# Performance work log

Measured on AMD Instinct MI355X. Metric: run time of the kernel, lower is better.

## Reference

```python
import jax, jax.numpy as jnp
import numpy as np

C_GMS = 0.0026  # constant c in the GMS map


def _median3(x):
    # 3x3 median with zero padding (matches kornia MedianBlur: conv2d-unfold
    # with zero padding, then median of the 9 values; odd count so torch's
    # lower-median == true median). x: [B,1,H,W]
    B, C, H, W = x.shape
    xp = jnp.pad(x, ((0, 0), (0, 0), (1, 1), (1, 1)))
    patches = jnp.stack(
        [xp[:, :, i:i + H, j:j + W] for i in range(3) for j in range(3)], axis=0
    )  # [9,B,1,H,W]
    return jnp.median(patches, axis=0)


def _prewitt(x):
    # fixed 2-channel Prewitt conv, VALID padding, then gradient magnitude
    Gx = jnp.array([[-1., 0., 1.], [-1., 0., 1.], [-1., 0., 1.]], dtype=x.dtype) / 3.0
    Gy = jnp.array([[1., 1., 1.], [0., 0., 0.], [-1., -1., -1.]], dtype=x.dtype) / 3.0
    k = jnp.stack([Gx, Gy])[:, None]  # [2,1,3,3] OIHW
    g = jax.lax.conv_general_dilated(
        x, k, window_strides=(1, 1), padding='VALID',
        dimension_numbers=('NCHW', 'OIHW', 'NCHW'))  # [B,2,H-2,W-2]
    return jnp.sqrt(jnp.sum(g * g, axis=1, keepdims=True))


def _gms_loss(Ii, Ir):
    x = jnp.mean(Ii, axis=1, keepdims=True)  # channel mean -> grayscale
    y = jnp.mean(Ir, axis=1, keepdims=True)
    gI = _prewitt(_median3(x))
    gR = _prewitt(_median3(y))
    gmap = (2.0 * gI * gR + C_GMS) / (gI * gI + gR * gR + C_GMS)
    return jnp.mean(1.0 - gmap)


def _avg_pool2(x):
    # avg_pool2d(kernel=2, stride=2)
    B, C, H, W = x.shape
    return x.reshape(B, C, H // 2, 2, W // 2, 2).mean(axis=(3, 5))


def setup_inputs() -> dict:
    key = jax.random.key(0)
    k1, k2 = jax.random.split(key)
    Ii = jax.random.uniform(k1, (16, 3, 512, 512), dtype=jnp.float32)
    Ir = jax.random.uniform(k2, (16, 3, 512, 512), dtype=jnp.float32)
    return {"Ii": Ii, "Ir": Ir}


def reference(Ii, Ir):
    total = _gms_loss(Ii, Ir)
    for _ in range(3):  # fixed 4-scale pyramid
        Ii = _avg_pool2(Ii)
        Ir = _avg_pool2(Ir)
        total = total + _gms_loss(Ii, Ir)
    return total / 4.0
```

## Files before the change

kernel.cpp:

```cpp
#include <hip/hip_runtime.h>

#define C_GMS 0.0026f

__device__ __forceinline__ float dppL(float x) {
    return __int_as_float(__builtin_amdgcn_mov_dpp(__float_as_int(x), 0x138, 0xf, 0xf, true));
}
__device__ __forceinline__ float dppR(float x) {
    return __int_as_float(__builtin_amdgcn_mov_dpp(__float_as_int(x), 0x130, 0xf, 0xf, true));
}
__device__ __forceinline__ float med3f(float a, float b, float c) {
    return __builtin_amdgcn_fmed3f(a, b, c);
}

template<bool RGB, bool POOL, int RC>
__global__ __launch_bounds__(256) void gms_scale_kernel(
    const float* __restrict__ srcX, const float* __restrict__ srcY,
    int H, int W, int nstrips, int nchunks,
    float* __restrict__ partial,
    float* __restrict__ dX, float* __restrict__ dY)
{
    const int lane = threadIdx.x & 63;
    const int u = blockIdx.x * 4 + (threadIdx.x >> 6);

    const int s  = u % nstrips;
    const int t1 = u / nstrips;
    const int k  = t1 % nchunks;
    const int b  = t1 / nchunks;

    const int c0 = 60 * s - 1;
    const int c  = c0 + lane;
    const int R0 = k * RC;
    const int iend = min(R0 + RC, H - 2);

    const int HW = H * W;
    const float* PX = srcX + (size_t)b * (RGB ? 3 * HW : HW);
    const float* PY = srcY + (size_t)b * (RGB ? 3 * HW : HW);
    const bool cok = (c >= 0) && (c < W);

    auto loadrow2 = [&](int r, float& vx, float& vy) {
        vx = 0.0f; vy = 0.0f;
        if (r >= 0 && r < H) {
            if (cok) {
                int o = r * W + c;
                if (RGB) {
                    vx = (PX[o] + PX[o + HW] + PX[o + 2 * HW]) * (1.0f / 3.0f);
                    vy = (PY[o] + PY[o + HW] + PY[o + 2 * HW]) * (1.0f / 3.0f);
                } else {
                    vx = PX[o];
                    vy = PY[o];
                }
            }
        }
    };

    auto medrow = [&](float ga, float gb, float gc, float& m, float& rs) {
        float lo = fminf(fminf(ga, gb), gc);
        float me = med3f(ga, gb, gc);
        float hi = fmaxf(fmaxf(ga, gb), gc);
        float lmax = fmaxf(fmaxf(dppL(lo), lo), dppR(lo));
        float mid  = med3f(dppL(me), me, dppR(me));
        float hmin = fminf(fminf(dppL(hi), hi), dppR(hi));
        m  = med3f(lmax, mid, hmin);
        rs = m + dppL(m) + dppR(m);
    };

    const int Hd = H >> 1, Wd = W >> 1;
    const int phalf = R0 >> 1;
    const int pend  = min(phalf + (RC >> 1), Hd);
    const bool poolLane = ((lane & 1) == 1) && (lane <= 59) && (c + 1 < W);

    auto dopool = [&](float bx, float cx, float by, float cy, int p) {
        if (!POOL) return;
        if (p < phalf || p >= pend) return;
        float ux = bx + cx, uy = by + cy;
        float hx = ux + dppR(ux);
        float hy = uy + dppR(uy);
        if (poolLane) {
            size_t o = ((size_t)b * Hd + p) * Wd + (c >> 1);
            dX[o] = hx * 0.25f;
            dY[o] = hy * 0.25f;
        }
    };

    float xa, ya, xb, yb, xc, yc, xd, yd, xe, ye;
    loadrow2(R0 - 1, xa, ya);
    loadrow2(R0,     xb, yb);
    loadrow2(R0 + 1, xc, yc);
    loadrow2(R0 + 2, xd, yd);
    loadrow2(R0 + 3, xe, ye);

    float mx0, mx1, mx2, rx0, rx1, rx2;
    float my0, my1, my2, ry0, ry1, ry2;
    medrow(xa, xb, xc, mx0, rx0); medrow(ya, yb, yc, my0, ry0);
    dopool(xb, xc, yb, yc, phalf);
    medrow(xb, xc, xd, mx1, rx1); medrow(yb, yc, yd, my1, ry1);
    medrow(xc, xd, xe, mx2, rx2); medrow(yc, yd, ye, my2, ry2);

    float gx2 = xd, gx3 = xe, gy2 = yd, gy3 = ye;

    const bool outLane = (lane >= 2) && (lane <= 61) && (c <= W - 2);
    float acc = 0.0f;

    for (int i = R0; i < iend; ++i) {
        float nx, ny;
        loadrow2(i + 4, nx, ny);

        float csx = mx0 + mx1 + mx2;
        float csy = my0 + my1 + my2;
        float Gxx = dppR(csx) - dppL(csx);
        float Gxy = dppR(csy) - dppL(csy);
        float Gyx = rx0 - rx2;
        float Gyy = ry0 - ry2;
        float gI = sqrtf(Gxx * Gxx + Gyx * Gyx) * (1.0f / 3.0f);
        float gR = sqrtf(Gxy * Gxy + Gyy * Gyy) * (1.0f / 3.0f);
        float gmap = (2.0f * gI * gR + C_GMS) / (gI * gI + gR * gR + C_GMS);
        if (outLane) acc += 1.0f - gmap;

        if (((i + 3) & 1) == 1) dopool(gx2, gx3, gy2, gy3, (i + 2) >> 1);

        float mxn, rxn, myn, ryn;
        medrow(gx2, gx3, nx, mxn, rxn);
        medrow(gy2, gy3, ny, myn, ryn);
        mx0 = mx1; mx1 = mx2; mx2 = mxn; rx0 = rx1; rx1 = rx2; rx2 = rxn;
        my0 = my1; my1 = my2; my2 = myn; ry0 = ry1; ry1 = ry2; ry2 = ryn;
        gx2 = gx3; gx3 = nx; gy2 = gy3; gy3 = ny;
    }

    for (int off = 32; off; off >>= 1) acc += __shfl_down(acc, off, 64);
    if (lane == 0) partial[u] = acc;
}

__global__ __launch_bounds__(256) void finalize_kernel(
    const float* __restrict__ P, int n0, int n1, int n2, int n3,
    float* __restrict__ out)
{
    const int tid = threadIdx.x;
    const double w0 = 1.0 / (4.0 * 16.0 * 510.0 * 510.0);
    const double w1 = 1.0 / (4.0 * 16.0 * 254.0 * 254.0);
    const double w2 = 1.0 / (4.0 * 16.0 * 126.0 * 126.0);
    const double w3 = 1.0 / (4.0 * 16.0 * 62.0 * 62.0);
    const int e0 = n0, e1 = e0 + n1, e2 = e1 + n2, e3 = e2 + n3;
    double v = 0.0;
    for (int i = tid; i < e3; i += 256) {
        double w = (i < e0) ? w0 : (i < e1) ? w1 : (i < e2) ? w2 : w3;
        v += (double)P[i] * w;
    }
    for (int off = 32; off; off >>= 1) v += __shfl_down(v, off, 64);
    __shared__ double wsum[4];
    int lane = tid & 63, wid = tid >> 6;
    if (lane == 0) wsum[wid] = v;
    __syncthreads();
    if (tid == 0) out[0] = (float)(wsum[0] + wsum[1] + wsum[2] + wsum[3]);
}

extern "C" void kernel_launch(void* const* d_in, const int* in_sizes, int n_in,
                              void* d_out, int out_size, void* d_ws, size_t ws_size,
                              hipStream_t stream) {
    const float* Ii = (const float*)d_in[0];
    const float* Ir = (const float*)d_in[1];
    float* out = (float*)d_out;
    const int B = 16;

    const int n0 = B * 9 * 64;
    const int n1 = B * 5 * 32;
    const int n2 = B * 3 * 16;
    const int n3 = B * 2 * 8;

    char* ws = (char*)d_ws;
    float* P  = (float*)ws;
    float* X1 = P + 16384;
    float* Y1 = X1 + B * 256 * 256;
    float* X2 = Y1 + B * 256 * 256;
    float* Y2 = X2 + B * 128 * 128;
    float* X3 = Y2 + B * 128 * 128;
    float* Y3 = X3 + B * 64 * 64;

    gms_scale_kernel<true,  true,  8><<<n0 / 4, 256, 0, stream>>>(Ii, Ir, 512, 512, 9, 64, P, X1, Y1);
    gms_scale_kernel<false, true,  8><<<n1 / 4, 256, 0, stream>>>(X1, Y1, 256, 256, 5, 32, P + n0, X2, Y2);
    gms_scale_kernel<false, true,  8><<<n2 / 4, 256, 0, stream>>>(X2, Y2, 128, 128, 3, 16, P + n0 + n1, X3, Y3);
    gms_scale_kernel<false, false, 8><<<n3 / 4, 256, 0, stream>>>(X3, Y3, 64, 64, 2, 8, P + n0 + n1 + n2, nullptr, nullptr);

    finalize_kernel<<<1, 256, 0, stream>>>(P, n0, n1, n2, n3, out);
}
```

Before: 165.9 us.

## Fuse all pyramid scales into one kernel computing pooled gray directly from input

Replaces the four per-scale launches and the separate finalize kernel with a single launch. Each wave computes its scale's downsampled grayscale values directly from the full-resolution RGB inputs by averaging FxF blocks, so no pooled intermediates are written or read back. A last-block-done atomic counter performs the final weighted reduction inside the same kernel. This removes launch gaps and serialization between scales, but coarse scales now re-read far more input bytes per output pixel (up to 8x8x3 floats), and a memset launch is added.

After: 458.4 us. 2.76x slower.

```diff
diff --git a/kernel.cpp b/kernel.cpp
--- a/kernel.cpp
+++ b/kernel.cpp
@@ -12,44 +12,59 @@
     return __builtin_amdgcn_fmed3f(a, b, c);
 }
 
-template<bool RGB, bool POOL, int RC>
-__global__ __launch_bounds__(256) void gms_scale_kernel(
-    const float* __restrict__ srcX, const float* __restrict__ srcY,
-    int H, int W, int nstrips, int nchunks,
-    float* __restrict__ partial,
-    float* __restrict__ dX, float* __restrict__ dY)
+template<int F>
+__device__ __forceinline__ float grayval(const float* __restrict__ p, int r, int c) {
+    constexpr int HW = 512 * 512;
+    float s = 0.0f;
+    #pragma unroll 1
+    for (int fr = 0; fr < F; ++fr) {
+        const float* row = p + (size_t)(r * F + fr) * 512 + c * F;
+        #pragma unroll
+        for (int ch = 0; ch < 3; ++ch) {
+            const float* q = row + ch * HW;
+            if constexpr (F == 1) {
+                s += q[0];
+            } else if constexpr (F == 2) {
+                float2 t = *(const float2*)q; s += t.x + t.y;
+            } else if constexpr (F == 4) {
+                float4 t = *(const float4*)q; s += (t.x + t.y) + (t.z + t.w);
+            } else {
+                float4 t0 = *(const float4*)q;
+                float4 t1 = *(const float4*)(q + 4);
+                s += ((t0.x + t0.y) + (t0.z + t0.w)) + ((t1.x + t1.y) + (t1.z + t1.w));
+            }
+        }
+    }
+    return s * (1.0f / (3.0f * F * F));
+}
+
+template<int F>
+__device__ __forceinline__ void gms_phase(
+    int u, const float* __restrict__ Ii, const float* __restrict__ Ir,
+    int nstrips, int nchunks, float* __restrict__ partial)
 {
+    constexpr int Hk = 512 / F;
+    constexpr int RC = 8;
     const int lane = threadIdx.x & 63;
-    const int u = blockIdx.x * 4 + (threadIdx.x >> 6);
 
     const int s  = u % nstrips;
     const int t1 = u / nstrips;
     const int k  = t1 % nchunks;
     const int b  = t1 / nchunks;
 
-    const int c0 = 60 * s - 1;
-    const int c  = c0 + lane;
+    const int c  = 60 * s - 1 + lane;
     const int R0 = k * RC;
-    const int iend = min(R0 + RC, H - 2);
+    const int iend = min(R0 + RC, Hk - 2);
 
-    const int HW = H * W;
-    const float* PX = srcX + (size_t)b * (RGB ? 3 * HW : HW);
-    const float* PY = srcY + (size_t)b * (RGB ? 3 * HW : HW);
-    const bool cok = (c >= 0) && (c < W);
+    const float* PX = Ii + (size_t)b * 3 * 512 * 512;
+    const float* PY = Ir + (size_t)b * 3 * 512 * 512;
+    const bool cok = (c >= 0) && (c < Hk);
 
     auto loadrow2 = [&](int r, float& vx, float& vy) {
         vx = 0.0f; vy = 0.0f;
-        if (r >= 0 && r < H) {
-            if (cok) {
-                int o = r * W + c;
-                if (RGB) {
-                    vx = (PX[o] + PX[o + HW] + PX[o + 2 * HW]) * (1.0f / 3.0f);
-                    vy = (PY[o] + PY[o + HW] + PY[o + 2 * HW]) * (1.0f / 3.0f);
-                } else {
-                    vx = PX[o];
-                    vy = PY[o];
-                }
-            }
+        if (r >= 0 && r < Hk && cok) {
+            vx = grayval<F>(PX, r, c);
+            vy = grayval<F>(PY, r, c);
         }
     };
 
@@ -64,24 +79,6 @@
         rs = m + dppL(m) + dppR(m);
     };
 
-    const int Hd = H >> 1, Wd = W >> 1;
-    const int phalf = R0 >> 1;
-    const int pend  = min(phalf + (RC >> 1), Hd);
-    const bool poolLane = ((lane & 1) == 1) && (lane <= 59) && (c + 1 < W);
-
-    auto dopool = [&](float bx, float cx, float by, float cy, int p) {
-        if (!POOL) return;
-        if (p < phalf || p >= pend) return;
-        float ux = bx + cx, uy = by + cy;
-        float hx = ux + dppR(ux);
-        float hy = uy + dppR(uy);
-        if (poolLane) {
-            size_t o = ((size_t)b * Hd + p) * Wd + (c >> 1);
-            dX[o] = hx * 0.25f;
-            dY[o] = hy * 0.25f;
-        }
-    };
-
     float xa, ya, xb, yb, xc, yc, xd, yd, xe, ye;
     loadrow2(R0 - 1, xa, ya);
     loadrow2(R0,     xb, yb);
@@ -92,13 +89,12 @@
     float mx0, mx1, mx2, rx0, rx1, rx2;
     float my0, my1, my2, ry0, ry1, ry2;
     medrow(xa, xb, xc, mx0, rx0); medrow(ya, yb, yc, my0, ry0);
-    dopool(xb, xc, yb, yc, phalf);
     medrow(xb, xc, xd, mx1, rx1); medrow(yb, yc, yd, my1, ry1);
     medrow(xc, xd, xe, mx2, rx2); medrow(yc, yd, ye, my2, ry2);
 
     float gx2 = xd, gx3 = xe, gy2 = yd, gy3 = ye;
 
-    const bool outLane = (lane >= 2) && (lane <= 61) && (c <= W - 2);
+    const bool outLane = (lane >= 2) && (lane <= 61) && (c <= Hk - 2);
     float acc = 0.0f;
 
     for (int i = R0; i < iend; ++i) {
@@ -116,8 +112,6 @@
         float gmap = (2.0f * gI * gR + C_GMS) / (gI * gI + gR * gR + C_GMS);
         if (outLane) acc += 1.0f - gmap;
 
-        if (((i + 3) & 1) == 1) dopool(gx2, gx3, gy2, gy3, (i + 2) >> 1);
-
         float mxn, rxn, myn, ryn;
         medrow(gx2, gx3, nx, mxn, rxn);
         medrow(gy2, gy3, ny, myn, ryn);
@@ -127,28 +121,53 @@
     }
 
     for (int off = 32; off; off >>= 1) acc += __shfl_down(acc, off, 64);
-    if (lane == 0) partial[u] = acc;
+    if (lane == 0)
+        __hip_atomic_store(&partial[u], acc, __ATOMIC_RELAXED, __HIP_MEMORY_SCOPE_AGENT);
 }
 
-__global__ __launch_bounds__(256) void finalize_kernel(
-    const float* __restrict__ P, int n0, int n1, int n2, int n3,
+#define N0 9216
+#define N1 2560
+#define N2 768
+#define N3 256
+#define NTOT (N0 + N1 + N2 + N3)
+
+__global__ __launch_bounds__(256) void msgms_main(
+    const float* __restrict__ Ii, const float* __restrict__ Ir,
+    float* __restrict__ P, unsigned int* __restrict__ counter,
     float* __restrict__ out)
 {
+    const int u = blockIdx.x * 4 + (threadIdx.x >> 6);
+    if      (u < N0)                gms_phase<1>(u,                 Ii, Ir, 9, 64, P);
+    else if (u < N0 + N1)           gms_phase<2>(u - N0,            Ii, Ir, 5, 32, P + N0);
+    else if (u < N0 + N1 + N2)      gms_phase<4>(u - N0 - N1,       Ii, Ir, 3, 16, P + N0 + N1);
+    else                            gms_phase<8>(u - N0 - N1 - N2,  Ii, Ir, 2,  8, P + N0 + N1 + N2);
+
+    __shared__ int lastFlag;
+    __syncthreads();
+    if (threadIdx.x == 0) {
+        __threadfence();
+        unsigned int old = __hip_atomic_fetch_add(counter, 1u, __ATOMIC_ACQ_REL,
+                                                  __HIP_MEMORY_SCOPE_AGENT);
+        lastFlag = (old == (unsigned int)(gridDim.x - 1));
+    }
+    __syncthreads();
+    if (!lastFlag) return;
+
+    __threadfence();
     const int tid = threadIdx.x;
     const double w0 = 1.0 / (4.0 * 16.0 * 510.0 * 510.0);
     const double w1 = 1.0 / (4.0 * 16.0 * 254.0 * 254.0);
     const double w2 = 1.0 / (4.0 * 16.0 * 126.0 * 126.0);
     const double w3 = 1.0 / (4.0 * 16.0 * 62.0 * 62.0);
-    const int e0 = n0, e1 = e0 + n1, e2 = e1 + n2, e3 = e2 + n3;
     double v = 0.0;
-    for (int i = tid; i < e3; i += 256) {
-        double w = (i < e0) ? w0 : (i < e1) ? w1 : (i < e2) ? w2 : w3;
-        v += (double)P[i] * w;
+    for (int i = tid; i < NTOT; i += 256) {
+        float p = __hip_atomic_load(&P[i], __ATOMIC_RELAXED, __HIP_MEMORY_SCOPE_AGENT);
+        double w = (i < N0) ? w0 : (i < N0 + N1) ? w1 : (i < N0 + N1 + N2) ? w2 : w3;
+        v += (double)p * w;
     }
     for (int off = 32; off; off >>= 1) v += __shfl_down(v, off, 64);
     __shared__ double wsum[4];
-    int lane = tid & 63, wid = tid >> 6;
-    if (lane == 0) wsum[wid] = v;
+    if ((tid & 63) == 0) wsum[tid >> 6] = v;
     __syncthreads();
     if (tid == 0) out[0] = (float)(wsum[0] + wsum[1] + wsum[2] + wsum[3]);
 }
@@ -159,26 +178,12 @@
     const float* Ii = (const float*)d_in[0];
     const float* Ir = (const float*)d_in[1];
     float* out = (float*)d_out;
-    const int B = 16;
-
-    const int n0 = B * 9 * 64;
-    const int n1 = B * 5 * 32;
-    const int n2 = B * 3 * 16;
-    const int n3 = B * 2 * 8;
 
     char* ws = (char*)d_ws;
-    float* P  = (float*)ws;
-    float* X1 = P + 16384;
-    float* Y1 = X1 + B * 256 * 256;
-    float* X2 = Y1 + B * 256 * 256;
-    float* Y2 = X2 + B * 128 * 128;
-    float* X3 = Y2 + B * 128 * 128;
-    float* Y3 = X3 + B * 64 * 64;
+    unsigned int* counter = (unsigned int*)ws;
+    float* P = (float*)(ws + 256);
 
-    gms_scale_kernel<true,  true,  8><<<n0 / 4, 256, 0, stream>>>(Ii, Ir, 512, 512, 9, 64, P, X1, Y1);
-    gms_scale_kernel<false, true,  8><<<n1 / 4, 256, 0, stream>>>(X1, Y1, 256, 256, 5, 32, P + n0, X2, Y2);
-    gms_scale_kernel<false, true,  8><<<n2 / 4, 256, 0, stream>>>(X2, Y2, 128, 128, 3, 16, P + n0 + n1, X3, Y3);
-    gms_scale_kernel<false, false, 8><<<n3 / 4, 256, 0, stream>>>(X3, Y3, 64, 64, 2, 8, P + n0 + n1 + n2, nullptr, nullptr);
+    hipMemsetAsync(counter, 0, 256, stream);
 
-    finalize_kernel<<<1, 256, 0, stream>>>(P, n0, n1, n2, n3, out);
+    msgms_main<<<NTOT / 4, 256, 0, stream>>>(Ii, Ir, P, counter, out);
 }
```
